# Kernel tuning notes

Hardware: AMD Instinct MI355X
Metric: run time of the kernel (lower is better)

Reference implementation:

```python
import jax, jax.numpy as jnp
import numpy as np

N_USERS = 4096
N_ITEMS = 4096
D = 64  # embedding_dim / out_features
N = N_USERS + N_ITEMS
ALPHA = 0.2  # LeakyReLU slope
NEG_INF = jnp.float32(-9e15)


def setup_inputs() -> dict:
    key = jax.random.key(0)
    ks = jax.random.split(key, 11)
    s = 0.05  # xavier-ish scale
    rn = lambda k, shape: jax.random.normal(k, shape, jnp.float32) * s
    adj = jax.random.randint(ks[0], (N, N), 0, 2, jnp.int32)
    return {
        "adj": adj,
        "user_emb": rn(ks[1], (N_USERS, D)),
        "item_emb": rn(ks[2], (N_ITEMS, D)),
        "W0_w": rn(ks[3], (D, D)), "W0_b": rn(ks[4], (D,)), "a0": rn(ks[5], (2 * D, 1)),
        "W1_w": rn(ks[6], (D, D)), "W1_b": rn(ks[7], (D,)), "a1": rn(ks[8], (2 * D, 1)),
        "out_w": rn(ks[9], (D, D)), "out_b": rn(ks[10], (D,)),
    }


def gat_layer(x, adj, W_w, W_b, a):
    # Wh: [N, D]
    Wh = x @ W_w.T + W_b
    # Original materializes [N,N,2D] concat then matmul with a.
    # Algebraically identical: e_ij = leakyrelu(a1 . Wh_i + a2 . Wh_j)
    src = Wh @ a[:D]          # [N, 1] -> row contribution
    dst = (Wh @ a[D:]).T      # [1, N] -> column contribution
    e = jax.nn.leaky_relu(src + dst, ALPHA)        # [N, N]
    e = jnp.where(adj > 0, e, NEG_INF)
    att = jax.nn.softmax(e, axis=1)                # dropout=0.0 (eval)
    return att @ Wh                                 # [N, D]


def reference(adj, user_emb, item_emb, W0_w, W0_b, a0, W1_w, W1_b, a1, out_w, out_b):
    x = jnp.concatenate([user_emb, item_emb], axis=0)  # [N, D]
    x = jax.nn.relu(gat_layer(x, adj, W0_w, W0_b, a0))
    x = jax.nn.relu(gat_layer(x, adj, W1_w, W1_b, a1))
    u, it = x[:N_USERS], x[N_USERS:]
    return (u @ out_w.T + out_b, it @ out_w.T + out_b)
```

## Files before the change

kernel.cpp:

```cpp
#include <hip/hip_runtime.h>


typedef __attribute__((ext_vector_type(8))) __bf16 bf16x8;
typedef __attribute__((ext_vector_type(4))) float  f32x4;

union Frag {
    bf16x8         v;
    unsigned int   w[4];
    unsigned short h[8];
};

__device__ __forceinline__ unsigned short f2bf(float f) {
    unsigned int u = __float_as_uint(f);
    u += 0x7FFFu + ((u >> 16) & 1u);
    return (unsigned short)(u >> 16);
}

__device__ __forceinline__ void prep_tail(
    float (*xs)[65], float (*Wt)[65], float (*sred)[64], float (*dred)[64],
    const float* __restrict__ W, const float* __restrict__ bias,
    const float* __restrict__ avec,
    unsigned short* __restrict__ WhT, float* __restrict__ sraw,
    float* __restrict__ draw, int tid, int r0)
{
    for (int e = tid; e < 4096; e += 256) {
        int o = e >> 6, c = e & 63;
        Wt[c][o] = W[e];
    }
    __syncthreads();

    int r = tid & 63, chunk = tid >> 6, c0 = chunk * 16;
    float acc[16];
#pragma unroll
    for (int o = 0; o < 16; o++) acc[o] = bias[c0 + o];
    for (int c = 0; c < 64; c++) {
        float xv = xs[r][c];
#pragma unroll
        for (int o = 0; o < 16; o++) acc[o] += xv * Wt[c][c0 + o];
    }

    float sp = 0.f, dp = 0.f;
#pragma unroll
    for (int o = 0; o < 16; o++) {
        sp += acc[o] * avec[c0 + o];
        dp += acc[o] * avec[64 + c0 + o];
    }
    sred[chunk][r] = sp;
    dred[chunk][r] = dp;

#pragma unroll
    for (int o = 0; o < 16; o++)
        WhT[(c0 + o) * 8192 + r0 + r] = f2bf(acc[o]);

    __syncthreads();
    if (tid < 64) {
        int g = r0 + tid;
        sraw[g] = sred[0][tid] + sred[1][tid] + sred[2][tid] + sred[3][tid];
        draw[g] = dred[0][tid] + dred[1][tid] + dred[2][tid] + dred[3][tid];
    }
}

__global__ __launch_bounds__(256) void k_prep0(
    const float* __restrict__ ue, const float* __restrict__ ie,
    const float* __restrict__ W, const float* __restrict__ bias,
    const float* __restrict__ avec,
    unsigned short* __restrict__ WhT,
    float* __restrict__ sraw, float* __restrict__ draw)
{
    __shared__ float xs[64][65];
    __shared__ float Wt[64][65];
    __shared__ float sred[4][64];
    __shared__ float dred[4][64];
    int tid = threadIdx.x, r0 = blockIdx.x * 64;

    for (int e = tid; e < 4096; e += 256) {
        int r = e >> 6, c = e & 63;
        int row = r0 + r;
        xs[r][c] = (row < 4096) ? ue[row * 64 + c] : ie[(row - 4096) * 64 + c];
    }
    prep_tail(xs, Wt, sred, dred, W, bias, avec, WhT, sraw, draw, tid, r0);
}

template <int NS>
__global__ __launch_bounds__(256) void k_prep1(
    const float* __restrict__ numP, const float* __restrict__ denP,
    const float* __restrict__ W, const float* __restrict__ bias,
    const float* __restrict__ avec,
    unsigned short* __restrict__ WhT,
    float* __restrict__ sraw, float* __restrict__ draw)
{
    __shared__ float xs[64][65];
    __shared__ float Wt[64][65];
    __shared__ float sred[4][64];
    __shared__ float dred[4][64];
    __shared__ float dtot[64];
    int tid = threadIdx.x, r0 = blockIdx.x * 64;

    if (tid < 64) {
        float s = 0.f;
#pragma unroll
        for (int p = 0; p < NS; p++) s += denP[p * 8192 + r0 + tid];
        dtot[tid] = fmaxf(s, 1e-20f);
    }
    __syncthreads();
    for (int e = tid; e < 4096; e += 256) {
        int r = e >> 6, c = e & 63;
        float s = 0.f;
#pragma unroll
        for (int p = 0; p < NS; p++)
            s += numP[(size_t)p * 524288 + (r0 + r) * 64 + c];
        float v = s / dtot[r];
        xs[r][c] = v > 0.f ? v : 0.f;
    }
    prep_tail(xs, Wt, sred, dred, W, bias, avec, WhT, sraw, draw, tid, r0);
}

template <int RAW, int NSPLIT>
__global__ __launch_bounds__(256, 8) void k_agg(
    const int* __restrict__ adj, unsigned int* __restrict__ adjbits,
    const unsigned short* __restrict__ WhT,
    const float* __restrict__ sraw, const float* __restrict__ draw,
    float* __restrict__ numP, float* __restrict__ denP)
{
    const int KR = 8192 / NSPLIT;
    int tid  = threadIdx.x;
    int wave = tid >> 6, lane = tid & 63;
    int quad = lane >> 4, l16 = lane & 15;
    int rowblk = blockIdx.x, ks = blockIdx.y;
    int row = rowblk * 64 + wave * 16 + l16;
    int k0  = ks * KR;

    float sv = sraw[row];

    f32x4 accs[4];
    f32x4 accd = {0.f, 0.f, 0.f, 0.f};
#pragma unroll
    for (int nt = 0; nt < 4; nt++) accs[nt] = accd;

    Frag ones;
    ones.w[0] = ones.w[1] = ones.w[2] = ones.w[3] = 0x3F803F80u;

    for (int kb = k0; kb < k0 + KR; kb += 32) {
        int kq = kb + quad * 8;

        unsigned int mask8;
        if constexpr (RAW) {
            const int4* ap = reinterpret_cast<const int4*>(adj + (size_t)row * 8192 + kq);
            int4 a0 = ap[0], a1 = ap[1];
            int ai[8] = {a0.x, a0.y, a0.z, a0.w, a1.x, a1.y, a1.z, a1.w};
            mask8 = 0;
#pragma unroll
            for (int j = 0; j < 8; j++)
                if (ai[j] != 0) mask8 |= (1u << j);
            reinterpret_cast<unsigned char*>(adjbits)[(size_t)row * 1024 + (kb >> 3) + quad] =
                (unsigned char)mask8;
        } else {
            unsigned int word = adjbits[row * 256 + (kb >> 5)];
            mask8 = (word >> (quad * 8)) & 0xFFu;
        }

        float4 dd0 = *reinterpret_cast<const float4*>(draw + kq);
        float4 dd1 = *reinterpret_cast<const float4*>(draw + kq + 4);
        float dv[8] = {dd0.x, dd0.y, dd0.z, dd0.w, dd1.x, dd1.y, dd1.z, dd1.w};

        Frag A;
#pragma unroll
        for (int j = 0; j < 8; j++) {
            float t  = sv + dv[j];
            float lr = t > 0.f ? t : 0.2f * t;
            float w  = ((mask8 >> j) & 1u) ? __expf(lr) : 0.f;
            A.h[j] = f2bf(w);
        }

#pragma unroll
        for (int nt = 0; nt < 4; nt++) {
            Frag B;
            B.v = *reinterpret_cast<const bf16x8*>(WhT + (size_t)(nt * 16 + l16) * 8192 + kq);
            accs[nt] = __builtin_amdgcn_mfma_f32_16x16x32_bf16(A.v, B.v, accs[nt], 0, 0, 0);
        }
        accd = __builtin_amdgcn_mfma_f32_16x16x32_bf16(A.v, ones.v, accd, 0, 0, 0);
    }

    int rbase = rowblk * 64 + wave * 16 + quad * 4;
    size_t nb = (size_t)ks * 524288;
#pragma unroll
    for (int rr = 0; rr < 4; rr++) {
        if (l16 == 0) denP[ks * 8192 + rbase + rr] = accd[rr];
#pragma unroll
        for (int nt = 0; nt < 4; nt++)
            numP[nb + (size_t)(rbase + rr) * 64 + nt * 16 + l16] = accs[nt][rr];
    }
}

template <int NS>
__global__ __launch_bounds__(256) void k_out(
    const float* __restrict__ numP, const float* __restrict__ denP,
    const float* __restrict__ W, const float* __restrict__ bias,
    float* __restrict__ out)
{
    __shared__ float xs[64][65];
    __shared__ float Wt[64][65];
    __shared__ float dtot[64];
    int tid = threadIdx.x, r0 = blockIdx.x * 64;

    if (tid < 64) {
        float s = 0.f;
#pragma unroll
        for (int p = 0; p < NS; p++) s += denP[p * 8192 + r0 + tid];
        dtot[tid] = fmaxf(s, 1e-20f);
    }
    __syncthreads();
    for (int e = tid; e < 4096; e += 256) {
        int r = e >> 6, c = e & 63;
        float s = 0.f;
#pragma unroll
        for (int p = 0; p < NS; p++)
            s += numP[(size_t)p * 524288 + (r0 + r) * 64 + c];
        float v = s / dtot[r];
        xs[r][c] = v > 0.f ? v : 0.f;
    }
    for (int e = tid; e < 4096; e += 256) {
        int o = e >> 6, c = e & 63;
        Wt[c][o] = W[e];
    }
    __syncthreads();

    int r = tid & 63, chunk = tid >> 6, c0 = chunk * 16;
    float acc[16];
#pragma unroll
    for (int o = 0; o < 16; o++) acc[o] = bias[c0 + o];
    for (int c = 0; c < 64; c++) {
        float xv = xs[r][c];
#pragma unroll
        for (int o = 0; o < 16; o++) acc[o] += xv * Wt[c][c0 + o];
    }
#pragma unroll
    for (int o = 0; o < 16; o++)
        out[(r0 + r) * 64 + c0 + o] = acc[o];
}

extern "C" void kernel_launch(void* const* d_in, const int* in_sizes, int n_in,
                              void* d_out, int out_size, void* d_ws, size_t ws_size,
                              hipStream_t stream)
{
    const int*   adj = (const int*)d_in[0];
    const float* ue  = (const float*)d_in[1];
    const float* ie  = (const float*)d_in[2];
    const float* W0w = (const float*)d_in[3];
    const float* W0b = (const float*)d_in[4];
    const float* a0  = (const float*)d_in[5];
    const float* W1w = (const float*)d_in[6];
    const float* W1b = (const float*)d_in[7];
    const float* a1  = (const float*)d_in[8];
    const float* Ow  = (const float*)d_in[9];
    const float* Ob  = (const float*)d_in[10];

    constexpr int NS0 = 16, NS1 = 8;

    char* ws = (char*)d_ws;
    size_t off = 0;
    auto alloc = [&](size_t bytes) -> char* {
        char* p = ws + off;
        off += (bytes + 255) & ~(size_t)255;
        return p;
    };
    float*          numP    = (float*)alloc((size_t)NS0 * 524288 * 4);
    float*          denP    = (float*)alloc((size_t)NS0 * 8192 * 4);
    unsigned int*   adjbits = (unsigned int*)alloc(8192 * 1024);
    unsigned short* WhT0    = (unsigned short*)alloc(64 * 8192 * 2);
    unsigned short* WhT1    = (unsigned short*)alloc(64 * 8192 * 2);
    float* sr0 = (float*)alloc(8192 * 4);
    float* dr0 = (float*)alloc(8192 * 4);
    float* sr1 = (float*)alloc(8192 * 4);
    float* dr1 = (float*)alloc(8192 * 4);

    k_prep0<<<128, 256, 0, stream>>>(ue, ie, W0w, W0b, a0, WhT0, sr0, dr0);
    k_agg<1, NS0><<<dim3(128, NS0), 256, 0, stream>>>(adj, adjbits, WhT0,
                                                      sr0, dr0, numP, denP);
    k_prep1<NS0><<<128, 256, 0, stream>>>(numP, denP, W1w, W1b, a1, WhT1, sr1, dr1);
    k_agg<0, NS1><<<dim3(128, NS1), 256, 0, stream>>>((const int*)nullptr, adjbits, WhT1,
                                                      sr1, dr1, numP, denP);
    k_out<NS1><<<128, 256, 0, stream>>>(numP, denP, Ow, Ob, (float*)d_out);
}
```

Measured before the change: 573.1 us.

## Pack adjacency with ballot, factor exp into precomputed terms, prefetch agg operands

Adds a separate wave-ballot kernel that packs the int32 adjacency into a bitmask before layer 0. Both aggregation layers now read only these bits. The per-edge exp(leakyrelu(s+d)) is replaced by a product of per-node exponentials (exp(s)*exp(d) or exp(.2s)*exp(.2d)) computed in the prep kernels, which removes transcendental work from the inner loop. The aggregation loop also software-pipelines the mask, vector and WhT loads one step ahead, uses packed bf16x2 conversion, and runs layer 1 with 16 splits and occupancy hint 4. In exchange it adds more per-k loads, higher register pressure, and a risk of overflow or precision loss from factoring the exponentials.

```diff
diff --git a/kernel.cpp b/kernel.cpp
--- a/kernel.cpp
+++ b/kernel.cpp
@@ -1,4 +1,5 @@
 #include <hip/hip_runtime.h>
+#include <hip/hip_bf16.h>
 
 
 typedef __attribute__((ext_vector_type(8))) __bf16 bf16x8;
@@ -10,18 +11,50 @@
     unsigned short h[8];
 };
 
+union BF2 {
+    __hip_bfloat162 b;
+    unsigned int    u;
+};
+
 __device__ __forceinline__ unsigned short f2bf(float f) {
     unsigned int u = __float_as_uint(f);
     u += 0x7FFFu + ((u >> 16) & 1u);
     return (unsigned short)(u >> 16);
 }
 
+__global__ __launch_bounds__(256) void k_pack(
+    const int* __restrict__ adj, unsigned long long* __restrict__ bits)
+{
+    int wgid = blockIdx.x * 4 + (threadIdx.x >> 6);
+    int lane = threadIdx.x & 63;
+    const long long NW  = 2048LL * 4;
+    const long long TOT = 8192LL * 8192;
+    for (long long base = (long long)wgid * 256; base < TOT; base += NW * 256) {
+        int a0 = adj[base + lane];
+        int a1 = adj[base +  64 + lane];
+        int a2 = adj[base + 128 + lane];
+        int a3 = adj[base + 192 + lane];
+        unsigned long long m0 = __ballot(a0 != 0);
+        unsigned long long m1 = __ballot(a1 != 0);
+        unsigned long long m2 = __ballot(a2 != 0);
+        unsigned long long m3 = __ballot(a3 != 0);
+        if (lane == 0) {
+            ulonglong2* p = reinterpret_cast<ulonglong2*>(bits + (base >> 6));
+            p[0] = ulonglong2{m0, m1};
+            p[1] = ulonglong2{m2, m3};
+        }
+    }
+}
+
 __device__ __forceinline__ void prep_tail(
     float (*xs)[65], float (*Wt)[65], float (*sred)[64], float (*dred)[64],
     const float* __restrict__ W, const float* __restrict__ bias,
     const float* __restrict__ avec,
-    unsigned short* __restrict__ WhT, float* __restrict__ sraw,
-    float* __restrict__ draw, int tid, int r0)
+    unsigned short* __restrict__ WhT,
+    float* __restrict__ sraw, float* __restrict__ draw,
+    float* __restrict__ E1, float* __restrict__ E2,
+    float* __restrict__ F1, float* __restrict__ F2,
+    int tid, int r0)
 {
     for (int e = tid; e < 4096; e += 256) {
         int o = e >> 6, c = e & 63;
@@ -55,8 +88,10 @@
     __syncthreads();
     if (tid < 64) {
         int g = r0 + tid;
-        sraw[g] = sred[0][tid] + sred[1][tid] + sred[2][tid] + sred[3][tid];
-        draw[g] = dred[0][tid] + dred[1][tid] + dred[2][tid] + dred[3][tid];
+        float s = sred[0][tid] + sred[1][tid] + sred[2][tid] + sred[3][tid];
+        float d = dred[0][tid] + dred[1][tid] + dred[2][tid] + dred[3][tid];
+        sraw[g] = s;  E1[g] = __expf(s);  E2[g] = __expf(0.2f * s);
+        draw[g] = d;  F1[g] = __expf(d);  F2[g] = __expf(0.2f * d);
     }
 }
 
@@ -65,7 +100,9 @@
     const float* __restrict__ W, const float* __restrict__ bias,
     const float* __restrict__ avec,
     unsigned short* __restrict__ WhT,
-    float* __restrict__ sraw, float* __restrict__ draw)
+    float* __restrict__ sraw, float* __restrict__ draw,
+    float* __restrict__ E1, float* __restrict__ E2,
+    float* __restrict__ F1, float* __restrict__ F2)
 {
     __shared__ float xs[64][65];
     __shared__ float Wt[64][65];
@@ -78,7 +115,8 @@
         int row = r0 + r;
         xs[r][c] = (row < 4096) ? ue[row * 64 + c] : ie[(row - 4096) * 64 + c];
     }
-    prep_tail(xs, Wt, sred, dred, W, bias, avec, WhT, sraw, draw, tid, r0);
+    prep_tail(xs, Wt, sred, dred, W, bias, avec, WhT, sraw, draw,
+              E1, E2, F1, F2, tid, r0);
 }
 
 template <int NS>
@@ -87,7 +125,9 @@
     const float* __restrict__ W, const float* __restrict__ bias,
     const float* __restrict__ avec,
     unsigned short* __restrict__ WhT,
-    float* __restrict__ sraw, float* __restrict__ draw)
+    float* __restrict__ sraw, float* __restrict__ draw,
+    float* __restrict__ E1, float* __restrict__ E2,
+    float* __restrict__ F1, float* __restrict__ F2)
 {
     __shared__ float xs[64][65];
     __shared__ float Wt[64][65];
@@ -112,17 +152,46 @@
         float v = s / dtot[r];
         xs[r][c] = v > 0.f ? v : 0.f;
     }
-    prep_tail(xs, Wt, sred, dred, W, bias, avec, WhT, sraw, draw, tid, r0);
-}
-
-template <int RAW, int NSPLIT>
-__global__ __launch_bounds__(256, 8) void k_agg(
-    const int* __restrict__ adj, unsigned int* __restrict__ adjbits,
+    prep_tail(xs, Wt, sred, dred, W, bias, avec, WhT, sraw, draw,
+              E1, E2, F1, F2, tid, r0);
+}
+
+struct KData {
+    unsigned int mask;
+    float4 dv0, dv1, f10, f11, f20, f21;
+    Frag   B[4];
+};
+
+__device__ __forceinline__ void load_kdata(
+    KData& kd, int row, int kb, int quad, int l16,
+    const unsigned int* __restrict__ bits32,
+    const float* __restrict__ draw,
+    const float* __restrict__ F1v, const float* __restrict__ F2v,
+    const unsigned short* __restrict__ WhT)
+{
+    int kq = kb + quad * 8;
+    kd.mask = bits32[row * 256 + (kb >> 5)];
+    kd.dv0 = *reinterpret_cast<const float4*>(draw + kq);
+    kd.dv1 = *reinterpret_cast<const float4*>(draw + kq + 4);
+    kd.f10 = *reinterpret_cast<const float4*>(F1v + kq);
+    kd.f11 = *reinterpret_cast<const float4*>(F1v + kq + 4);
+    kd.f20 = *reinterpret_cast<const float4*>(F2v + kq);
+    kd.f21 = *reinterpret_cast<const float4*>(F2v + kq + 4);
+#pragma unroll
+    for (int nt = 0; nt < 4; nt++)
+        kd.B[nt].v = *reinterpret_cast<const bf16x8*>(
+            WhT + (size_t)(nt * 16 + l16) * 8192 + kq);
+}
+
+__device__ __forceinline__ void agg_body(
+    const unsigned int* __restrict__ bits32,
     const unsigned short* __restrict__ WhT,
     const float* __restrict__ sraw, const float* __restrict__ draw,
+    const float* __restrict__ E1v, const float* __restrict__ E2v,
+    const float* __restrict__ F1v, const float* __restrict__ F2v,
     float* __restrict__ numP, float* __restrict__ denP)
 {
-    const int KR = 8192 / NSPLIT;
+    const int KR = 512;
     int tid  = threadIdx.x;
     int wave = tid >> 6, lane = tid & 63;
     int quad = lane >> 4, l16 = lane & 15;
@@ -130,7 +199,7 @@
     int row = rowblk * 64 + wave * 16 + l16;
     int k0  = ks * KR;
 
-    float sv = sraw[row];
+    float sv = sraw[row], e1 = E1v[row], e2 = E2v[row];
 
     f32x4 accs[4];
     f32x4 accd = {0.f, 0.f, 0.f, 0.f};
@@ -140,45 +209,45 @@
     Frag ones;
     ones.w[0] = ones.w[1] = ones.w[2] = ones.w[3] = 0x3F803F80u;
 
+    KData cur, nxt;
+    load_kdata(cur, row, k0, quad, l16, bits32, draw, F1v, F2v, WhT);
+
     for (int kb = k0; kb < k0 + KR; kb += 32) {
-        int kq = kb + quad * 8;
-
-        unsigned int mask8;
-        if constexpr (RAW) {
-            const int4* ap = reinterpret_cast<const int4*>(adj + (size_t)row * 8192 + kq);
-            int4 a0 = ap[0], a1 = ap[1];
-            int ai[8] = {a0.x, a0.y, a0.z, a0.w, a1.x, a1.y, a1.z, a1.w};
-            mask8 = 0;
-#pragma unroll
-            for (int j = 0; j < 8; j++)
-                if (ai[j] != 0) mask8 |= (1u << j);
-            reinterpret_cast<unsigned char*>(adjbits)[(size_t)row * 1024 + (kb >> 3) + quad] =
-                (unsigned char)mask8;
-        } else {
-            unsigned int word = adjbits[row * 256 + (kb >> 5)];
-            mask8 = (word >> (quad * 8)) & 0xFFu;
+        int kbn = (kb + 32 < k0 + KR) ? kb + 32 : k0;
+        load_kdata(nxt, row, kbn, quad, l16, bits32, draw, F1v, F2v, WhT);
+
+        unsigned int mask8 = (cur.mask >> (quad * 8)) & 0xFFu;
+        float dva[8] = {cur.dv0.x, cur.dv0.y, cur.dv0.z, cur.dv0.w,
+                        cur.dv1.x, cur.dv1.y, cur.dv1.z, cur.dv1.w};
+        float f1a[8] = {cur.f10.x, cur.f10.y, cur.f10.z, cur.f10.w,
+                        cur.f11.x, cur.f11.y, cur.f11.z, cur.f11.w};
+        float f2a[8] = {cur.f20.x, cur.f20.y, cur.f20.z, cur.f20.w,
+                        cur.f21.x, cur.f21.y, cur.f21.z, cur.f21.w};
+
+        Frag A;
+#pragma unroll
+        for (int p = 0; p < 4; p++) {
+            float w2[2];
+#pragma unroll
+            for (int h = 0; h < 2; h++) {
+                int j = 2 * p + h;
+                float t   = sv + dva[j];
+                bool  neg = t < 0.f;
+                float ww  = (neg ? e2 : e1) * (neg ? f2a[j] : f1a[j]);
+                w2[h] = ((mask8 >> j) & 1u) ? ww : 0.f;
+            }
+            BF2 cv;
+            cv.b = __float22bfloat162_rn(float2{w2[0], w2[1]});
+            A.w[p] = cv.u;
         }
 
-        float4 dd0 = *reinterpret_cast<const float4*>(draw + kq);
-        float4 dd1 = *reinterpret_cast<const float4*>(draw + kq + 4);
-        float dv[8] = {dd0.x, dd0.y, dd0.z, dd0.w, dd1.x, dd1.y, dd1.z, dd1.w};
-
-        Frag A;
-#pragma unroll
-        for (int j = 0; j < 8; j++) {
-            float t  = sv + dv[j];
-            float lr = t > 0.f ? t : 0.2f * t;
-            float w  = ((mask8 >> j) & 1u) ? __expf(lr) : 0.f;
-            A.h[j] = f2bf(w);
-        }
-
-#pragma unroll
-        for (int nt = 0; nt < 4; nt++) {
-            Frag B;
-            B.v = *reinterpret_cast<const bf16x8*>(WhT + (size_t)(nt * 16 + l16) * 8192 + kq);
-            accs[nt] = __builtin_amdgcn_mfma_f32_16x16x32_bf16(A.v, B.v, accs[nt], 0, 0, 0);
-        }
+#pragma unroll
+        for (int nt = 0; nt < 4; nt++)
+            accs[nt] = __builtin_amdgcn_mfma_f32_16x16x32_bf16(A.v, cur.B[nt].v,
+                                                               accs[nt], 0, 0, 0);
         accd = __builtin_amdgcn_mfma_f32_16x16x32_bf16(A.v, ones.v, accd, 0, 0, 0);
+
+        cur = nxt;
     }
 
     int rbase = rowblk * 64 + wave * 16 + quad * 4;
@@ -190,6 +259,26 @@
         for (int nt = 0; nt < 4; nt++)
             numP[nb + (size_t)(rbase + rr) * 64 + nt * 16 + l16] = accs[nt][rr];
     }
+}
+
+__global__ __launch_bounds__(256, 4) void k_agg_l0(
+    const unsigned int* __restrict__ bits32, const unsigned short* __restrict__ WhT,
+    const float* __restrict__ sraw, const float* __restrict__ draw,
+    const float* __restrict__ E1v, const float* __restrict__ E2v,
+    const float* __restrict__ F1v, const float* __restrict__ F2v,
+    float* __restrict__ numP, float* __restrict__ denP)
+{
+    agg_body(bits32, WhT, sraw, draw, E1v, E2v, F1v, F2v, numP, denP);
+}
+
+__global__ __launch_bounds__(256, 4) void k_agg_l1(
+    const unsigned int* __restrict__ bits32, const unsigned short* __restrict__ WhT,
+    const float* __restrict__ sraw, const float* __restrict__ draw,
+    const float* __restrict__ E1v, const float* __restrict__ E2v,
+    const float* __restrict__ F1v, const float* __restrict__ F2v,
+    float* __restrict__ numP, float* __restrict__ denP)
+{
+    agg_body(bits32, WhT, sraw, draw, E1v, E2v, F1v, F2v, numP, denP);
 }
 
 template <int NS>
@@ -255,7 +344,7 @@
     const float* Ow  = (const float*)d_in[9];
     const float* Ob  = (const float*)d_in[10];
 
-    constexpr int NS0 = 16, NS1 = 8;
+    constexpr int NS = 16;
 
     char* ws = (char*)d_ws;
     size_t off = 0;
@@ -264,21 +353,29 @@
         off += (bytes + 255) & ~(size_t)255;
         return p;
     };
-    float*          numP    = (float*)alloc((size_t)NS0 * 524288 * 4);
-    float*          denP    = (float*)alloc((size_t)NS0 * 8192 * 4);
-    unsigned int*   adjbits = (unsigned int*)alloc(8192 * 1024);
+    float*          numP    = (float*)alloc((size_t)NS * 524288 * 4);
+    float*          denP    = (float*)alloc((size_t)NS * 8192 * 4);
+    unsigned long long* adjbits = (unsigned long long*)alloc(8192 * 1024);
     unsigned short* WhT0    = (unsigned short*)alloc(64 * 8192 * 2);
     unsigned short* WhT1    = (unsigned short*)alloc(64 * 8192 * 2);
-    float* sr0 = (float*)alloc(8192 * 4);
-    float* dr0 = (float*)alloc(8192 * 4);
-    float* sr1 = (float*)alloc(8192 * 4);
-    float* dr1 = (float*)alloc(8192 * 4);
-
-    k_prep0<<<128, 256, 0, stream>>>(ue, ie, W0w, W0b, a0, WhT0, sr0, dr0);
-    k_agg<1, NS0><<<dim3(128, NS0), 256, 0, stream>>>(adj, adjbits, WhT0,
-                                                      sr0, dr0, numP, denP);
-    k_prep1<NS0><<<128, 256, 0, stream>>>(numP, denP, W1w, W1b, a1, WhT1, sr1, dr1);
-    k_agg<0, NS1><<<dim3(128, NS1), 256, 0, stream>>>((const int*)nullptr, adjbits, WhT1,
-                                                      sr1, dr1, numP, denP);
-    k_out<NS1><<<128, 256, 0, stream>>>(numP, denP, Ow, Ob, (float*)d_out);
-}
+    float* sr0 = (float*)alloc(8192 * 4); float* dr0 = (float*)alloc(8192 * 4);
+    float* E10 = (float*)alloc(8192 * 4); float* E20 = (float*)alloc(8192 * 4);
+    float* F10 = (float*)alloc(8192 * 4); float* F20 = (float*)alloc(8192 * 4);
+    float* sr1 = (float*)alloc(8192 * 4); float* dr1 = (float*)alloc(8192 * 4);
+    float* E11 = (float*)alloc(8192 * 4); float* E21 = (float*)alloc(8192 * 4);
+    float* F11 = (float*)alloc(8192 * 4); float* F21 = (float*)alloc(8192 * 4);
+
+    const unsigned int* bits32 = (const unsigned int*)adjbits;
+
+    k_pack<<<2048, 256, 0, stream>>>(adj, adjbits);
+
+    k_prep0<<<128, 256, 0, stream>>>(ue, ie, W0w, W0b, a0, WhT0,
+                                     sr0, dr0, E10, E20, F10, F20);
+    k_agg_l0<<<dim3(128, NS), 256, 0, stream>>>(bits32, WhT0, sr0, dr0,
+                                                E10, E20, F10, F20, numP, denP);
+    k_prep1<NS><<<128, 256, 0, stream>>>(numP, denP, W1w, W1b, a1, WhT1,
+                                         sr1, dr1, E11, E21, F11, F21);
+    k_agg_l1<<<dim3(128, NS), 256, 0, stream>>>(bits32, WhT1, sr1, dr1,
+                                                E11, E21, F11, F21, numP, denP);
+    k_out<NS><<<128, 256, 0, stream>>>(numP, denP, Ow, Ob, (float*)d_out);
+}
```

Result: slower. 640.2 us (+11.7%).
